# Kernel optimization log

Hardware: AMD Instinct MI355X
Metric: run time of the kernel (lower is better)

Reference implementation:

```python
import jax, jax.numpy as jnp
import numpy as np
from jax import lax

FILTER_SIZE = 3
C_IN = 128
C_OUT = 256
PAD = 1
STRIDE = 1


def setup_inputs() -> dict:
    key = jax.random.key(0)
    k1, k2 = jax.random.split(key)
    prev_a = jax.random.normal(k1, (32, 56, 56, C_IN), dtype=jnp.float32)
    # filter_w initialized ~ N(0, 1) as in the original tf.random.normal
    filter_w = jax.random.normal(k2, (FILTER_SIZE, FILTER_SIZE, C_IN, C_OUT), dtype=jnp.float32)
    filter_b = jnp.zeros((1, 1, 1, C_OUT), dtype=jnp.float32)
    return {"prev_a": prev_a, "filter_w": filter_w, "filter_b": filter_b}


def reference(prev_a, filter_w, filter_b):
    # NHWC input, HWIO filter -> NHWC output; same math as the nested-loop conv:
    # z[i,h,w,c] = sum(prev_a_pad[i, h*s:h*s+f, w*s:w*s+f, :] * W[:,:,:,c]) + b[c]
    z = lax.conv_general_dilated(
        prev_a,
        filter_w,
        window_strides=(STRIDE, STRIDE),
        padding=[(PAD, PAD), (PAD, PAD)],
        dimension_numbers=("NHWC", "HWIO", "NHWC"),
    )
    z = z + filter_b  # bias broadcast over (m, H, W)
    return jax.nn.relu(z)
```

## Files before the change

### kernel.cpp

```cpp
#include <hip/hip_runtime.h>
#include <hip/hip_bf16.h>


#define NIMG 32
#define HH 56
#define WW 56
#define PH 58
#define PW 58
#define CIN 128
#define COUT 256
#define KTOT 1152
#define PAD_ELEMS (NIMG * PH * PW * CIN)

#define BK 32
#define KITERS (KTOT / BK)

typedef __attribute__((ext_vector_type(8))) short bf16x8;
typedef __attribute__((ext_vector_type(4))) short s16x4;
typedef __attribute__((ext_vector_type(4))) float f32x4;

__device__ __forceinline__ short f2bf(float x) {
    union { __hip_bfloat16 b; short s; } u;
    u.b = __float2bfloat16(x);
    return u.s;
}

typedef const void __attribute__((address_space(1)))* gas1_t;
typedef void __attribute__((address_space(3)))* las3_t;
__device__ __forceinline__ void async16(short* lds, const short* g) {
    __builtin_amdgcn_global_load_lds((gas1_t)g, (las3_t)lds, 16, 0, 0);
}

__global__ __launch_bounds__(256) void pack_input(const float* __restrict__ in,
                                                  short* __restrict__ pad) {
    const int tid  = blockIdx.x * 256 + threadIdx.x;
    const int flat = tid * 8;
    const int c8   = flat & (CIN - 1);
    const int rest = flat >> 7;
    const int iw   = rest % PW;
    const int r2   = rest / PW;
    const int ih   = r2 % PH;
    const int img  = r2 / PH;
    bf16x8 v = (bf16x8)0;
    if (ih >= 1 && ih <= HH && iw >= 1 && iw <= WW) {
        const float* p = in + (((size_t)(img * HH + ih - 1) * WW + (iw - 1)) * CIN + c8);
        const float4 x0 = *(const float4*)p;
        const float4 x1 = *(const float4*)(p + 4);
        v.s0 = f2bf(x0.x); v.s1 = f2bf(x0.y); v.s2 = f2bf(x0.z); v.s3 = f2bf(x0.w);
        v.s4 = f2bf(x1.x); v.s5 = f2bf(x1.y); v.s6 = f2bf(x1.z); v.s7 = f2bf(x1.w);
    }
    *(bf16x8*)(pad + flat) = v;
}

__global__ __launch_bounds__(256) void pack_wgt(const float* __restrict__ w,
                                                short* __restrict__ wt) {
    __shared__ short tile[32][33];
    const int k0 = blockIdx.x * 32;
    const int n0 = blockIdx.y * 32;
    const int t  = threadIdx.x;
    {
        const int kl  = t >> 3;
        const int nl4 = (t & 7) * 4;
        const float4 x = *(const float4*)(w + (size_t)(k0 + kl) * COUT + n0 + nl4);
        tile[kl][nl4 + 0] = f2bf(x.x);
        tile[kl][nl4 + 1] = f2bf(x.y);
        tile[kl][nl4 + 2] = f2bf(x.z);
        tile[kl][nl4 + 3] = f2bf(x.w);
    }
    __syncthreads();
    {
        const int nl  = t >> 3;
        const int kl4 = (t & 7) * 4;
        s16x4 v;
        v.x = tile[kl4 + 0][nl];
        v.y = tile[kl4 + 1][nl];
        v.z = tile[kl4 + 2][nl];
        v.w = tile[kl4 + 3][nl];
        *(s16x4*)(wt + (size_t)(n0 + nl) * KTOT + k0 + kl4) = v;
    }
}

__global__ __launch_bounds__(256) void conv_mfma(const short* __restrict__ apad,
                                                 const short* __restrict__ bwt,
                                                 const float* __restrict__ bias,
                                                 float* __restrict__ out) {
    __shared__ short As0[128 * BK], As1[128 * BK];
    __shared__ short Bs0[128 * BK], Bs1[128 * BK];

    const int t  = threadIdx.x;
    const int l  = t & 63;
    const int w  = t >> 6;
    const int m0 = blockIdx.y * 128;
    const int n0 = blockIdx.x * 128;

    const int Lc = (t & 7) ^ ((t >> 3) & 7);
    const int kc = Lc & 3;
    int abase[2], bbase[2];
#pragma unroll
    for (int j = 0; j < 2; ++j) {
        const int r   = 2 * (t >> 3) + (Lc >> 2) + j * 64;
        const int m   = m0 + r;
        const int img = m / (HH * WW);
        const int rem = m - img * (HH * WW);
        const int oh  = rem / WW;
        const int ow  = rem - oh * WW;
        abase[j] = ((img * PH + oh) * PW + ow) * CIN + kc * 8;
        bbase[j] = (n0 + r) * KTOT + kc * 8;
    }

    f32x4 acc[4][4];
#pragma unroll
    for (int i = 0; i < 4; ++i)
#pragma unroll
        for (int j = 0; j < 4; ++j) { f32x4 z = {0.f, 0.f, 0.f, 0.f}; acc[i][j] = z; }

    const int wm = w & 1;
    const int wn = w >> 1;
    const int fr = l & 15;
    const int fq = l >> 4;

#define STAGE(KT, AS, BS) do {                                              \
        const int _fhw  = (KT) >> 2;                                        \
        const int _fh   = _fhw / 3;                                         \
        const int _fw   = _fhw - _fh * 3;                                   \
        const int _aoff = (_fh * PW + _fw) * CIN + ((KT) & 3) * 32;         \
        const int _boff = (KT) * BK;                                        \
        _Pragma("unroll")                                                   \
        for (int _j = 0; _j < 2; ++_j) {                                    \
            async16((AS) + (_j * 256 + w * 64) * 8, apad + abase[_j] + _aoff); \
            async16((BS) + (_j * 256 + w * 64) * 8, bwt + bbase[_j] + _boff); \
        }                                                                   \
    } while (0)

#define FRAG(BASE, R) \
    (*(const bf16x8*)((BASE) + (((R) >> 1) << 6) + \
     (((((R) & 1) << 2) | fq) ^ (((R) >> 1) & 7)) * 8))

#define COMPUTE(AS, BS) do {                                                \
        bf16x8 _af[4], _bf[4];                                              \
        _Pragma("unroll")                                                   \
        for (int _i = 0; _i < 4; ++_i) _af[_i] = FRAG(AS, wm * 64 + _i * 16 + fr); \
        _Pragma("unroll")                                                   \
        for (int _j = 0; _j < 4; ++_j) _bf[_j] = FRAG(BS, wn * 64 + _j * 16 + fr); \
        _Pragma("unroll")                                                   \
        for (int _i = 0; _i < 4; ++_i)                                      \
            _Pragma("unroll")                                               \
            for (int _j = 0; _j < 4; ++_j)                                  \
                acc[_i][_j] = __builtin_amdgcn_mfma_f32_16x16x32_bf16(      \
                    _af[_i], _bf[_j], acc[_i][_j], 0, 0, 0);                \
    } while (0)

    STAGE(0, As0, Bs0);
    for (int kt = 0; kt < KITERS; kt += 2) {
        __syncthreads();
        STAGE(kt + 1, As1, Bs1);
        COMPUTE(As0, Bs0);
        __syncthreads();
        if (kt + 2 < KITERS) STAGE(kt + 2, As0, Bs0);
        COMPUTE(As1, Bs1);
    }

#pragma unroll
    for (int j = 0; j < 4; ++j) {
        const int n  = n0 + wn * 64 + j * 16 + fr;
        const float bj = bias[n];
#pragma unroll
        for (int i = 0; i < 4; ++i) {
            const int mrow = m0 + wm * 64 + i * 16 + fq * 4;
#pragma unroll
            for (int r = 0; r < 4; ++r) {
                const float v = acc[i][j][r] + bj;
                out[(size_t)(mrow + r) * COUT + n] = v > 0.f ? v : 0.f;
            }
        }
    }
#undef STAGE
#undef FRAG
#undef COMPUTE
}

extern "C" void kernel_launch(void* const* d_in, const int* in_sizes, int n_in,
                              void* d_out, int out_size, void* d_ws, size_t ws_size,
                              hipStream_t stream) {
    const float* in   = (const float*)d_in[0];
    const float* wgt  = (const float*)d_in[1];
    const float* bias = (const float*)d_in[2];
    float* out = (float*)d_out;

    short* pad = (short*)d_ws;
    short* wt  = (short*)d_ws + PAD_ELEMS;

    pack_input<<<PAD_ELEMS / 8 / 256, 256, 0, stream>>>(in, pad);
    pack_wgt<<<dim3(KTOT / 32, COUT / 32), 256, 0, stream>>>(wgt, wt);

    dim3 grid(COUT / 128, (NIMG * HH * WW) / 128);
    conv_mfma<<<grid, 256, 0, stream>>>(pad, wt, bias, out);
}
```

Before: 221.7 us.

## Use 4-stage LDS ring with register-prefetched fragments and swizzled block order

Replaces the double-buffered LDS loop with a four-buffer ring that keeps three async global-to-LDS stages in flight, uses explicit vmcnt waits plus raw barriers in place of __syncthreads, and double-buffers MFMA fragments in registers so LDS reads overlap compute. It also remaps the 1D grid so blocks sharing M tiles run close together for better L2 reuse of the activation tiles, and adds a launch bound of 2 blocks per CU. The aim is to hide global load latency and barrier stalls in the main loop. In exchange LDS use doubles to 64 KB per block and the hand-written waitcnt counts must match exactly how many loads are outstanding.

```diff
diff --git a/kernel.cpp b/kernel.cpp
--- a/kernel.cpp
+++ b/kernel.cpp
@@ -11,9 +11,8 @@
 #define COUT 256
 #define KTOT 1152
 #define PAD_ELEMS (NIMG * PH * PW * CIN)
-
 #define BK 32
-#define KITERS (KTOT / BK)
+#define KITERS 36
 
 typedef __attribute__((ext_vector_type(8))) short bf16x8;
 typedef __attribute__((ext_vector_type(4))) short s16x4;
@@ -80,18 +79,20 @@
     }
 }
 
-__global__ __launch_bounds__(256) void conv_mfma(const short* __restrict__ apad,
-                                                 const short* __restrict__ bwt,
-                                                 const float* __restrict__ bias,
-                                                 float* __restrict__ out) {
-    __shared__ short As0[128 * BK], As1[128 * BK];
-    __shared__ short Bs0[128 * BK], Bs1[128 * BK];
-
-    const int t  = threadIdx.x;
-    const int l  = t & 63;
-    const int w  = t >> 6;
-    const int m0 = blockIdx.y * 128;
-    const int n0 = blockIdx.x * 128;
+__global__ __launch_bounds__(256, 2) void conv_mfma(const short* __restrict__ apad,
+                                                    const short* __restrict__ bwt,
+                                                    const float* __restrict__ bias,
+                                                    float* __restrict__ out) {
+    __shared__ short As[4][128 * BK];
+    __shared__ short Bs[4][128 * BK];
+
+    const int t = threadIdx.x;
+    const int l = t & 63;
+    const int w = t >> 6;
+
+    const int L  = blockIdx.x;
+    const int m0 = (((L >> 4) << 3) | (L & 7)) * 128;
+    const int n0 = ((L >> 3) & 1) * 128;
 
     const int Lc = (t & 7) ^ ((t >> 3) & 7);
     const int kc = Lc & 3;
@@ -119,46 +120,79 @@
     const int fr = l & 15;
     const int fq = l >> 4;
 
-#define STAGE(KT, AS, BS) do {                                              \
-        const int _fhw  = (KT) >> 2;                                        \
-        const int _fh   = _fhw / 3;                                         \
-        const int _fw   = _fhw - _fh * 3;                                   \
-        const int _aoff = (_fh * PW + _fw) * CIN + ((KT) & 3) * 32;         \
-        const int _boff = (KT) * BK;                                        \
-        _Pragma("unroll")                                                   \
-        for (int _j = 0; _j < 2; ++_j) {                                    \
-            async16((AS) + (_j * 256 + w * 64) * 8, apad + abase[_j] + _aoff); \
-            async16((BS) + (_j * 256 + w * 64) * 8, bwt + bbase[_j] + _boff); \
-        }                                                                   \
+#define STAGE(KT) do {                                                        \
+        const int _b    = (KT) & 3;                                           \
+        const int _fhw  = (KT) >> 2;                                          \
+        const int _fh   = _fhw / 3;                                           \
+        const int _fw   = _fhw - _fh * 3;                                     \
+        const int _aoff = (_fh * PW + _fw) * CIN + ((KT) & 3) * 32;           \
+        const int _boff = (KT) * BK;                                          \
+        _Pragma("unroll")                                                     \
+        for (int _j = 0; _j < 2; ++_j) {                                      \
+            async16(&As[_b][(_j * 256 + w * 64) * 8], apad + abase[_j] + _aoff); \
+            async16(&Bs[_b][(_j * 256 + w * 64) * 8], bwt + bbase[_j] + _boff);  \
+        }                                                                     \
     } while (0)
 
 #define FRAG(BASE, R) \
     (*(const bf16x8*)((BASE) + (((R) >> 1) << 6) + \
      (((((R) & 1) << 2) | fq) ^ (((R) >> 1) & 7)) * 8))
 
-#define COMPUTE(AS, BS) do {                                                \
-        bf16x8 _af[4], _bf[4];                                              \
-        _Pragma("unroll")                                                   \
-        for (int _i = 0; _i < 4; ++_i) _af[_i] = FRAG(AS, wm * 64 + _i * 16 + fr); \
-        _Pragma("unroll")                                                   \
-        for (int _j = 0; _j < 4; ++_j) _bf[_j] = FRAG(BS, wn * 64 + _j * 16 + fr); \
-        _Pragma("unroll")                                                   \
-        for (int _i = 0; _i < 4; ++_i)                                      \
-            _Pragma("unroll")                                               \
-            for (int _j = 0; _j < 4; ++_j)                                  \
-                acc[_i][_j] = __builtin_amdgcn_mfma_f32_16x16x32_bf16(      \
-                    _af[_i], _bf[_j], acc[_i][_j], 0, 0, 0);                \
-    } while (0)
-
-    STAGE(0, As0, Bs0);
-    for (int kt = 0; kt < KITERS; kt += 2) {
-        __syncthreads();
-        STAGE(kt + 1, As1, Bs1);
-        COMPUTE(As0, Bs0);
-        __syncthreads();
-        if (kt + 2 < KITERS) STAGE(kt + 2, As0, Bs0);
-        COMPUTE(As1, Bs1);
-    }
+#define READF(KT, AF, BF) do {                                                \
+        const short* _as = As[(KT) & 3];                                      \
+        const short* _bs = Bs[(KT) & 3];                                      \
+        _Pragma("unroll")                                                     \
+        for (int _i = 0; _i < 4; ++_i) (AF)[_i] = FRAG(_as, wm * 64 + _i * 16 + fr); \
+        _Pragma("unroll")                                                     \
+        for (int _j = 0; _j < 4; ++_j) (BF)[_j] = FRAG(_bs, wn * 64 + _j * 16 + fr); \
+    } while (0)
+
+#define COMPUTE(AF, BF) do {                                                  \
+        _Pragma("unroll")                                                     \
+        for (int _i = 0; _i < 4; ++_i)                                        \
+            _Pragma("unroll")                                                 \
+            for (int _j = 0; _j < 4; ++_j)                                    \
+                acc[_i][_j] = __builtin_amdgcn_mfma_f32_16x16x32_bf16(        \
+                    (AF)[_i], (BF)[_j], acc[_i][_j], 0, 0, 0);                \
+    } while (0)
+
+#define WAIT4_BAR() do {                                                      \
+        asm volatile("s_waitcnt vmcnt(4) lgkmcnt(0)" ::: "memory");           \
+        asm volatile("s_barrier" ::: "memory");                               \
+    } while (0)
+#define WAIT0_BAR() do {                                                      \
+        asm volatile("s_waitcnt vmcnt(0) lgkmcnt(0)" ::: "memory");           \
+        asm volatile("s_barrier" ::: "memory");                               \
+    } while (0)
+
+    bf16x8 a0[4], b0[4], a1[4], b1[4];
+
+    STAGE(0); STAGE(1); STAGE(2);
+    asm volatile("s_waitcnt vmcnt(8)" ::: "memory");
+    asm volatile("s_barrier" ::: "memory");
+    READF(0, a0, b0);
+
+    for (int kt = 0; kt < 32; kt += 2) {
+        WAIT4_BAR();
+        STAGE(kt + 3);
+        READF(kt + 1, a1, b1);
+        COMPUTE(a0, b0);
+        WAIT4_BAR();
+        STAGE(kt + 4);
+        READF(kt + 2, a0, b0);
+        COMPUTE(a1, b1);
+    }
+    WAIT4_BAR();
+    STAGE(35);
+    READF(33, a1, b1);
+    COMPUTE(a0, b0);
+    WAIT4_BAR();
+    READF(34, a0, b0);
+    COMPUTE(a1, b1);
+    WAIT0_BAR();
+    READF(35, a1, b1);
+    COMPUTE(a0, b0);
+    COMPUTE(a1, b1);
 
 #pragma unroll
     for (int j = 0; j < 4; ++j) {
@@ -176,7 +210,10 @@
     }
 #undef STAGE
 #undef FRAG
+#undef READF
 #undef COMPUTE
+#undef WAIT4_BAR
+#undef WAIT0_BAR
 }
 
 extern "C" void kernel_launch(void* const* d_in, const int* in_sizes, int n_in,
@@ -193,6 +230,5 @@
     pack_input<<<PAD_ELEMS / 8 / 256, 256, 0, stream>>>(in, pad);
     pack_wgt<<<dim3(KTOT / 32, COUT / 32), 256, 0, stream>>>(wgt, wt);
 
-    dim3 grid(COUT / 128, (NIMG * HH * WW) / 128);
-    conv_mfma<<<grid, 256, 0, stream>>>(pad, wt, bias, out);
-}
+    conv_mfma<<<1568, 256, 0, stream>>>(pad, wt, bias, out);
+}
```

After: 232.6 us. 4.9% more time.
